# Performance work log

Measured on AMD Instinct MI355X. Metric: run time of the kernel, lower is better.

## Reference

```python
import jax, jax.numpy as jnp
import numpy as np

N = 100000

def _norm_edges(edge_index, n):
    # add self loops, compute symmetric GCN normalization
    loop = jnp.arange(n, dtype=edge_index.dtype)
    src = jnp.concatenate([edge_index[0], loop])
    dst = jnp.concatenate([edge_index[1], loop])
    deg = jax.ops.segment_sum(jnp.ones_like(dst, dtype=jnp.float32), dst, num_segments=n)
    dinv = jnp.where(deg > 0, deg ** -0.5, 0.0)
    norm = dinv[src] * dinv[dst]
    return src, dst, norm

def _gcn(x, W, b, src, dst, norm, n):
    h = x @ W  # [N, out]
    msg = h[src] * norm[:, None]
    return jax.ops.segment_sum(msg, dst, num_segments=n) + b

def setup_inputs() -> dict:
    key = jax.random.key(0)
    ks = jax.random.split(key, 20)
    E = 3200000
    d_in, d_out = 64, 64
    def w(k, i, o):
        return jax.random.normal(k, (i, o), dtype=jnp.float32) * (1.0 / np.sqrt(i))
    return {
        "x": jax.random.normal(ks[0], (N, d_in), dtype=jnp.float32),
        "t": jax.random.normal(ks[1], (N,), dtype=jnp.float32),
        "edge_index": jax.random.randint(ks[2], (2, E), 0, N, dtype=jnp.int64),
        "W1": w(ks[3], d_in + 1, 64), "b1": jnp.zeros((64,), jnp.float32),
        "W2": w(ks[4], 64, 128), "b2": jnp.zeros((128,), jnp.float32),
        "W3": w(ks[5], 128, 256), "b3": jnp.zeros((256,), jnp.float32),
        "W4": w(ks[6], 256, 128), "b4": jnp.zeros((128,), jnp.float32),
        "F1": w(ks[7], 128, 256), "c1": jnp.zeros((256,), jnp.float32),
        "F2": w(ks[8], 256, 128), "c2": jnp.zeros((128,), jnp.float32),
        "F3": w(ks[9], 128, d_out), "c3": jnp.zeros((d_out,), jnp.float32),
    }

def reference(x, t, edge_index, W1, b1, W2, b2, W3, b3, W4, b4, F1, c1, F2, c2, F3, c3):
    n = x.shape[0]
    src, dst, norm = _norm_edges(edge_index, n)
    h = jnp.concatenate([x, t[:, None]], axis=1)
    h = jax.nn.gelu(_gcn(h, W1, b1, src, dst, norm, n))
    h = jax.nn.gelu(_gcn(h, W2, b2, src, dst, norm, n))
    h = jax.nn.gelu(_gcn(h, W3, b3, src, dst, norm, n))
    h = jax.nn.gelu(_gcn(h, W4, b4, src, dst, norm, n))
    h = jax.nn.gelu(h @ F1 + c1)
    h = jax.nn.gelu(h @ F2 + c2)
    return h @ F3 + c3
```

## Files before the change

### kernel.cpp

```cpp
#include <hip/hip_runtime.h>

static constexpr int BLK = 256;

typedef double d2 __attribute__((ext_vector_type(2)));

__device__ __forceinline__ double gelu_d(double v){
  double u = 0.7978845608028654 * (v + 0.044715 * v * v * v);
  return 0.5 * v * (1.0 + tanh(u));
}

__global__ void zero_k(int* __restrict__ a, int n){
  int stride = gridDim.x * blockDim.x;
  for (int i = blockIdx.x*blockDim.x + threadIdx.x; i < n; i += stride) a[i] = 0;
}

__global__ void detect_k(const int* __restrict__ ei, int* __restrict__ flag){
  if (threadIdx.x == 0 && blockIdx.x == 0){
    int zeros = 0;
    for (int i = 0; i < 64; ++i) if (ei[2*i + 1] == 0) ++zeros;
    *flag = (zeros >= 48) ? 1 : 0;
  }
}

__global__ void count_k(const int* __restrict__ ei, int E, const int* __restrict__ flag,
                        int* __restrict__ cnt){
  int is64 = *flag;
  int stride = gridDim.x * blockDim.x;
  for (int e = blockIdx.x*blockDim.x + threadIdx.x; e < E; e += stride){
    int d = is64 ? ei[2*(E + e)] : ei[E + e];
    atomicAdd(&cnt[d], 1);
  }
}

__global__ void dinv_k(const int* __restrict__ cnt, double* __restrict__ dinv, int n){
  int i = blockIdx.x*blockDim.x + threadIdx.x;
  if (i < n){
    double deg = (double)(cnt[i] + 1);
    dinv[i] = 1.0 / sqrt(deg);
  }
}

__global__ __launch_bounds__(256)
void scanA_k(const int* __restrict__ cnt, int* __restrict__ partial, int n, int chunk){
  __shared__ int red[256];
  int b = blockIdx.x;
  int lo = b * chunk, hi = min(n, lo + chunk);
  int s = 0;
  for (int i = lo + threadIdx.x; i < hi; i += 256) s += cnt[i];
  red[threadIdx.x] = s; __syncthreads();
  for (int off = 128; off > 0; off >>= 1){
    if (threadIdx.x < off) red[threadIdx.x] += red[threadIdx.x + off];
    __syncthreads();
  }
  if (threadIdx.x == 0) partial[b] = red[0];
}

__global__ __launch_bounds__(256)
void scanB_k(int* __restrict__ partial, int nb){
  __shared__ int sd[256];
  int tid = threadIdx.x;
  int v = (tid < nb) ? partial[tid] : 0;
  sd[tid] = v; __syncthreads();
  for (int off = 1; off < 256; off <<= 1){
    int t = (tid >= off) ? sd[tid - off] : 0;
    __syncthreads();
    sd[tid] += t;
    __syncthreads();
  }
  if (tid < nb) partial[tid] = sd[tid] - v;
  if (tid == 255) partial[nb] = sd[255];
}

__global__ __launch_bounds__(256)
void scanC_k(const int* __restrict__ cnt, const int* __restrict__ partial,
             int* __restrict__ rp, int n, int chunk, int nb){
  __shared__ int sd[256];
  int b = blockIdx.x;
  int lo = b * chunk, hi = min(n, lo + chunk);
  int run = partial[b];
  for (int base = lo; base < hi; base += 256){
    int i = base + threadIdx.x;
    int v = (i < hi) ? cnt[i] : 0;
    sd[threadIdx.x] = v; __syncthreads();
    for (int off = 1; off < 256; off <<= 1){
      int t = (threadIdx.x >= off) ? sd[threadIdx.x - off] : 0;
      __syncthreads();
      sd[threadIdx.x] += t;
      __syncthreads();
    }
    if (i < hi) rp[i] = run + sd[threadIdx.x] - v;
    run += sd[255];
    __syncthreads();
  }
  if (b == 0 && threadIdx.x == 0) rp[n] = partial[nb];
}

__global__ void scatter_k(const int* __restrict__ ei, int E, const int* __restrict__ flag,
                          const int* __restrict__ rp, int* __restrict__ fill,
                          const double* __restrict__ dinv,
                          int* __restrict__ col, double* __restrict__ val){
  int is64 = *flag;
  int stride = gridDim.x * blockDim.x;
  for (int e = blockIdx.x*blockDim.x + threadIdx.x; e < E; e += stride){
    int s = is64 ? ei[2*e]       : ei[e];
    int d = is64 ? ei[2*(E + e)] : ei[E + e];
    int p = rp[d] + atomicAdd(&fill[d], 1);
    col[p] = s;
    if (val) val[p] = dinv[s];
  }
}

template<typename ST>
__global__ void concat_k(const float* __restrict__ x, const float* __restrict__ t,
                         ST* __restrict__ h0, int n){
  int total = n * 66;
  int stride = gridDim.x * blockDim.x;
  for (int idx = blockIdx.x*blockDim.x + threadIdx.x; idx < total; idx += stride){
    int row = idx / 66;
    int c = idx - row * 66;
    float v = (c < 64) ? x[row*64 + c] : (c == 64 ? t[row] : 0.0f);
    h0[idx] = (ST)v;
  }
}

template<typename ST>
__global__ __launch_bounds__(256, 2)
void gemm_k(const ST* __restrict__ A, int K, int lda,
            const float* __restrict__ W, int NOUT,
            const float* __restrict__ bias,
            ST* __restrict__ C, float* __restrict__ Cf,
            int n, int fuse)
{
  __shared__ __align__(16) double As[128][34];
  __shared__ __align__(16) double Ws[32][66];
  int row0 = blockIdx.x * 128;
  int col0 = blockIdx.y * 64;
  int tid = threadIdx.x;
  int tr = tid >> 4, tc = tid & 15;
  int c0 = 2 * tc;
  double acc[8][4] = {};
  int ktiles = (K + 31) / 32;
  for (int kt = 0; kt < ktiles; ++kt){
    int k0 = kt * 32;
    {
      int r  = tid >> 1;
      int kk = (tid & 1) * 16;
      int gr = row0 + r;
      if constexpr (sizeof(ST) == 8){
        if (gr < n){
          const double* Ap = (const double*)A + (size_t)gr * lda + k0 + kk;
          #pragma unroll
          for (int g = 0; g < 8; ++g){
            d2 v = *(const d2*)(Ap + 2*g);
            *(d2*)&As[r][kk + 2*g] = v;
          }
        } else {
          #pragma unroll
          for (int g = 0; g < 8; ++g){ d2 z = {0.0, 0.0}; *(d2*)&As[r][kk + 2*g] = z; }
        }
      } else {
        const ST* Ap = A + (size_t)gr * lda + k0 + kk;
        #pragma unroll
        for (int u = 0; u < 16; ++u){
          int kg = k0 + kk + u;
          As[r][kk + u] = (gr < n && kg < K) ? (double)Ap[u] : 0.0;
        }
      }
    }
    {
      int r = tid >> 3;
      int c = (tid & 7) * 8;
      int kg = k0 + r;
      if (kg < K){
        const float* Wp = W + (size_t)kg * NOUT + col0 + c;
        #pragma unroll
        for (int g = 0; g < 4; ++g){
          d2 v; v.x = (double)Wp[2*g]; v.y = (double)Wp[2*g + 1];
          *(d2*)&Ws[r][c + 2*g] = v;
        }
      } else {
        #pragma unroll
        for (int g = 0; g < 4; ++g){ d2 z = {0.0, 0.0}; *(d2*)&Ws[r][c + 2*g] = z; }
      }
    }
    __syncthreads();
    #pragma unroll
    for (int kk = 0; kk < 32; kk += 2){
      d2 w0a = *(const d2*)&Ws[kk    ][c0];
      d2 w0b = *(const d2*)&Ws[kk    ][c0 + 32];
      d2 w1a = *(const d2*)&Ws[kk + 1][c0];
      d2 w1b = *(const d2*)&Ws[kk + 1][c0 + 32];
      #pragma unroll
      for (int i = 0; i < 8; ++i){
        d2 av = *(const d2*)&As[tr + 16*i][kk];
        acc[i][0] = fma(av.x, w0a.x, acc[i][0]);
        acc[i][1] = fma(av.x, w0a.y, acc[i][1]);
        acc[i][2] = fma(av.x, w0b.x, acc[i][2]);
        acc[i][3] = fma(av.x, w0b.y, acc[i][3]);
        acc[i][0] = fma(av.y, w1a.x, acc[i][0]);
        acc[i][1] = fma(av.y, w1a.y, acc[i][1]);
        acc[i][2] = fma(av.y, w1b.x, acc[i][2]);
        acc[i][3] = fma(av.y, w1b.y, acc[i][3]);
      }
    }
    __syncthreads();
  }
  #pragma unroll
  for (int i = 0; i < 8; ++i){
    int r = row0 + tr + 16*i;
    if (r >= n) continue;
    #pragma unroll
    for (int j = 0; j < 4; ++j){
      int c = col0 + ((j < 2) ? (c0 + j) : (c0 + 30 + j));
      double v = acc[i][j];
      if (fuse){ v += (double)bias[c]; if (fuse == 1) v = gelu_d(v); }
      if (fuse == 2) __builtin_nontemporal_store((float)v, &Cf[(size_t)r * NOUT + c]);
      else           __builtin_nontemporal_store((ST)v,   &C [(size_t)r * NOUT + c]);
    }
  }
}

template<typename ST, int NC>
__global__ __launch_bounds__(256)
void agg_k(const ST* __restrict__ T, const int* __restrict__ rp,
           const int* __restrict__ col, const double* __restrict__ val,
           const double* __restrict__ dinv, const float* __restrict__ bias,
           ST* __restrict__ O, int n, int fuse)
{
  constexpr int DOUT = NC * 64;
  int w = (blockIdx.x * blockDim.x + threadIdx.x) >> 6;
  int lane = threadIdx.x & 63;
  if (w >= n) return;
  double dv = dinv[w];
  const ST* Ti = T + (size_t)w * DOUT;
  double acc[NC];
  #pragma unroll
  for (int c = 0; c < NC; ++c) acc[c] = dv * (double)Ti[lane + 64*c];
  int e  = rp[w];
  int e1 = rp[w + 1];
  if (val){
    for (; e + 4 <= e1; e += 4){
      int s0 = __builtin_nontemporal_load(&col[e]);
      int s1 = __builtin_nontemporal_load(&col[e+1]);
      int s2 = __builtin_nontemporal_load(&col[e+2]);
      int s3 = __builtin_nontemporal_load(&col[e+3]);
      double v0 = __builtin_nontemporal_load(&val[e]);
      double v1 = __builtin_nontemporal_load(&val[e+1]);
      double v2 = __builtin_nontemporal_load(&val[e+2]);
      double v3 = __builtin_nontemporal_load(&val[e+3]);
      const ST* T0 = T + (size_t)s0 * DOUT;
      const ST* T1 = T + (size_t)s1 * DOUT;
      const ST* T2 = T + (size_t)s2 * DOUT;
      const ST* T3 = T + (size_t)s3 * DOUT;
      double t0[NC], t1[NC], t2[NC], t3[NC];
      #pragma unroll
      for (int c = 0; c < NC; ++c){
        t0[c] = (double)T0[lane + 64*c];
        t1[c] = (double)T1[lane + 64*c];
        t2[c] = (double)T2[lane + 64*c];
        t3[c] = (double)T3[lane + 64*c];
      }
      #pragma unroll
      for (int c = 0; c < NC; ++c){
        acc[c] = fma(v0, t0[c], acc[c]);
        acc[c] = fma(v1, t1[c], acc[c]);
        acc[c] = fma(v2, t2[c], acc[c]);
        acc[c] = fma(v3, t3[c], acc[c]);
      }
    }
    for (; e < e1; ++e){
      int s = __builtin_nontemporal_load(&col[e]);
      double v = __builtin_nontemporal_load(&val[e]);
      const ST* Ts = T + (size_t)s * DOUT;
      #pragma unroll
      for (int c = 0; c < NC; ++c) acc[c] = fma(v, (double)Ts[lane + 64*c], acc[c]);
    }
  } else {
    for (; e < e1; ++e){
      int s = col[e];
      double v = dinv[s];
      const ST* Ts = T + (size_t)s * DOUT;
      #pragma unroll
      for (int c = 0; c < NC; ++c) acc[c] = fma(v, (double)Ts[lane + 64*c], acc[c]);
    }
  }
  ST* Oi = O + (size_t)w * DOUT;
  #pragma unroll
  for (int c = 0; c < NC; ++c){
    double v = dv * acc[c];
    if (fuse) v = gelu_d(v + (double)bias[lane + 64*c]);
    __builtin_nontemporal_store((ST)v, &Oi[lane + 64*c]);
  }
}

template<typename ST>
static void run_net(const float* x, const float* t,
                    const float* W1, const float* b1, const float* W2, const float* b2,
                    const float* W3, const float* b3, const float* W4, const float* b4,
                    const float* F1, const float* c1, const float* F2, const float* c2,
                    const float* F3, const float* c3,
                    ST* b256, ST* ba, ST* bb,
                    const int* rp, const int* col, const double* val, const double* dinv,
                    float* out, int N, hipStream_t stream)
{
  auto gemm = [&](const ST* A, int K, int lda, const float* W, int NOUT, const float* bias,
                  ST* C, float* Cf, int fuse){
    dim3 g((N + 127) / 128, NOUT / 64);
    gemm_k<ST><<<g, dim3(BLK), 0, stream>>>(A, K, lda, W, NOUT, bias, C, Cf, N, fuse);
  };
  int aggGrid = (N * 64 + BLK - 1) / BLK;
  auto agg64 = [&](const ST* T, const float* bias, ST* O, int fuse){
    agg_k<ST,1><<<dim3(aggGrid), dim3(BLK), 0, stream>>>(T, rp, col, val, dinv, bias, O, N, fuse);
  };
  auto agg128 = [&](const ST* T, const float* bias, ST* O, int fuse){
    agg_k<ST,2><<<dim3(aggGrid), dim3(BLK), 0, stream>>>(T, rp, col, val, dinv, bias, O, N, fuse);
  };

  concat_k<ST><<<dim3(1024), dim3(BLK), 0, stream>>>(x, t, ba, N);
  gemm(ba, 65, 66, W1, 64, nullptr, bb, nullptr, 0);
  agg64(bb, b1, ba, 1);
  agg64(ba, nullptr, bb, 0);
  gemm(bb, 64, 64, W2, 128, b2, ba, nullptr, 1);
  agg128(ba, nullptr, bb, 0);
  gemm(bb, 128, 128, W3, 256, b3, b256, nullptr, 1);
  gemm(b256, 256, 256, W4, 128, nullptr, ba, nullptr, 0);
  agg128(ba, b4, bb, 1);
  gemm(bb, 128, 128, F1, 256, c1, b256, nullptr, 1);
  gemm(b256, 256, 256, F2, 128, c2, ba, nullptr, 1);
  gemm(ba, 128, 128, F3, 64, c3, nullptr, out, 2);
}

extern "C" void kernel_launch(void* const* d_in, const int* in_sizes, int n_in,
                              void* d_out, int out_size, void* d_ws, size_t ws_size,
                              hipStream_t stream)
{
  const float* x  = (const float*)d_in[0];
  const float* t  = (const float*)d_in[1];
  const int*   ei = (const int*)d_in[2];
  const float* W1 = (const float*)d_in[3];  const float* b1 = (const float*)d_in[4];
  const float* W2 = (const float*)d_in[5];  const float* b2 = (const float*)d_in[6];
  const float* W3 = (const float*)d_in[7];  const float* b3 = (const float*)d_in[8];
  const float* W4 = (const float*)d_in[9];  const float* b4 = (const float*)d_in[10];
  const float* F1 = (const float*)d_in[11]; const float* c1 = (const float*)d_in[12];
  const float* F2 = (const float*)d_in[13]; const float* c2 = (const float*)d_in[14];
  const float* F3 = (const float*)d_in[15]; const float* c3 = (const float*)d_in[16];
  float* out = (float*)d_out;
  int N = in_sizes[0] / 64;
  int E = in_sizes[2] / 2;

  char* p = (char*)d_ws;
  auto alloc = [&](size_t b){ char* r = p; p += (b + 255) & ~(size_t)255; return (void*)r; };
  int*    flag    = (int*)alloc(4);
  int*    cnt     = (int*)alloc((size_t)N * 4);
  int*    fill    = (int*)alloc((size_t)N * 4);
  int*    rp      = (int*)alloc((size_t)(N + 1) * 4);
  int*    partial = (int*)alloc((size_t)257 * 4);
  int*    col     = (int*)alloc((size_t)E * 4);
  double* dinv    = (double*)alloc((size_t)N * 8);
  size_t base = (size_t)(p - (char*)d_ws);

  size_t slackB = 1024;
  size_t actElems = (size_t)N * 512;
  size_t valBytes = ((size_t)E * 8 + 255) & ~(size_t)255;
  bool f64val = ws_size >= base + valBytes + actElems * sizeof(double) + 3*slackB;
  bool f64ok  = f64val || ws_size >= base + actElems * sizeof(double) + 3*slackB;
  bool f32val = ws_size >= base + valBytes + actElems * sizeof(float) + 3*slackB;
  bool f32ok  = f32val || ws_size >= base + actElems * sizeof(float) + 3*slackB;
  if (!f32ok) return;

  double* val = nullptr;
  if ((f64ok && f64val) || (!f64ok && f32val)) val = (double*)alloc((size_t)E * 8);

  int nb = 256;
  int chunk = (N + nb - 1) / nb;
  zero_k<<<dim3(256), dim3(BLK), 0, stream>>>(cnt, N);
  zero_k<<<dim3(256), dim3(BLK), 0, stream>>>(fill, N);
  detect_k<<<1, 64, 0, stream>>>(ei, flag);
  count_k<<<dim3(4096), dim3(BLK), 0, stream>>>(ei, E, flag, cnt);
  dinv_k<<<dim3((N + BLK - 1) / BLK), dim3(BLK), 0, stream>>>(cnt, dinv, N);
  scanA_k<<<dim3(nb), dim3(256), 0, stream>>>(cnt, partial, N, chunk);
  scanB_k<<<dim3(1), dim3(256), 0, stream>>>(partial, nb);
  scanC_k<<<dim3(nb), dim3(256), 0, stream>>>(cnt, partial, rp, N, chunk, nb);
  scatter_k<<<dim3(4096), dim3(BLK), 0, stream>>>(ei, E, flag, rp, fill, dinv, col, val);

  if (f64ok){
    double* b256 = (double*)alloc((size_t)N * 256 * 8 + slackB);
    double* ba   = (double*)alloc((size_t)N * 128 * 8 + slackB);
    double* bb   = (double*)alloc((size_t)N * 128 * 8 + slackB);
    run_net<double>(x, t, W1, b1, W2, b2, W3, b3, W4, b4, F1, c1, F2, c2, F3, c3,
                    b256, ba, bb, rp, col, val, dinv, out, N, stream);
  } else {
    float* b256 = (float*)alloc((size_t)N * 256 * 4 + slackB);
    float* ba   = (float*)alloc((size_t)N * 128 * 4 + slackB);
    float* bb   = (float*)alloc((size_t)N * 128 * 4 + slackB);
    run_net<float>(x, t, W1, b1, W2, b2, W3, b3, W4, b4, F1, c1, F2, c2, F3, c3,
                   b256, ba, bb, rp, col, val, dinv, out, N, stream);
  }
}
```

Measured before the change: 2.525 ms.

## Register-prefetch next GEMM tile, XOR-swizzle A tile in LDS, raise occupancy hint

The FP64 GEMM kernel now loads the next k-tile of A and W into registers while computing on the current tile in LDS, overlapping global memory latency with FMA work. The A tile in shared memory uses an XOR swizzle on the column index to reduce LDS bank conflicts for the row-strided reads. The launch bounds hint goes from 2 to 3 blocks per CU. Prefetch registers (16 doubles plus 8 floats) add pressure that competes with the higher occupancy target and may cause spills.

```diff
diff --git a/kernel.cpp b/kernel.cpp
--- a/kernel.cpp
+++ b/kernel.cpp
@@ -124,66 +124,89 @@
 }
 
 template<typename ST>
-__global__ __launch_bounds__(256, 2)
+__global__ __launch_bounds__(256, 3)
 void gemm_k(const ST* __restrict__ A, int K, int lda,
             const float* __restrict__ W, int NOUT,
             const float* __restrict__ bias,
             ST* __restrict__ C, float* __restrict__ Cf,
             int n, int fuse)
 {
-  __shared__ __align__(16) double As[128][34];
+  __shared__ __align__(16) double As[128 * 34];
   __shared__ __align__(16) double Ws[32][66];
-  int row0 = blockIdx.x * 128;
-  int col0 = blockIdx.y * 64;
-  int tid = threadIdx.x;
-  int tr = tid >> 4, tc = tid & 15;
-  int c0 = 2 * tc;
+  const int row0 = blockIdx.x * 128;
+  const int col0 = blockIdx.y * 64;
+  const int tid = threadIdx.x;
+  const int tr = tid >> 4, tc = tid & 15;
+  const int c0 = 2 * tc;
+  const int rdx = 2 * (tr & 7);
   double acc[8][4] = {};
-  int ktiles = (K + 31) / 32;
-  for (int kt = 0; kt < ktiles; ++kt){
-    int k0 = kt * 32;
-    {
-      int r  = tid >> 1;
-      int kk = (tid & 1) * 16;
-      int gr = row0 + r;
-      if constexpr (sizeof(ST) == 8){
-        if (gr < n){
-          const double* Ap = (const double*)A + (size_t)gr * lda + k0 + kk;
-          #pragma unroll
-          for (int g = 0; g < 8; ++g){
-            d2 v = *(const d2*)(Ap + 2*g);
-            *(d2*)&As[r][kk + 2*g] = v;
-          }
-        } else {
-          #pragma unroll
-          for (int g = 0; g < 8; ++g){ d2 z = {0.0, 0.0}; *(d2*)&As[r][kk + 2*g] = z; }
-        }
-      } else {
-        const ST* Ap = A + (size_t)gr * lda + k0 + kk;
+
+  const int sar = tid >> 1;
+  const int sah = tid & 1;
+  const int arb = sar * 34;
+  const int arx = 2 * (sar & 7);
+  const int swr = tid >> 3;
+  const int swc = (tid & 7) * 8;
+
+  const int ktiles = (K + 31) / 32;
+
+  double ga[16];
+  float  gw[8];
+
+  auto loadA = [&](int k0){
+    int gr = row0 + sar;
+    if constexpr (sizeof(ST) == 8){
+      if (gr < n){
+        const double* Ap = (const double*)A + (size_t)gr * lda + k0 + sah * 16;
         #pragma unroll
-        for (int u = 0; u < 16; ++u){
-          int kg = k0 + kk + u;
-          As[r][kk + u] = (gr < n && kg < K) ? (double)Ap[u] : 0.0;
-        }
-      }
-    }
-    {
-      int r = tid >> 3;
-      int c = (tid & 7) * 8;
-      int kg = k0 + r;
-      if (kg < K){
-        const float* Wp = W + (size_t)kg * NOUT + col0 + c;
-        #pragma unroll
-        for (int g = 0; g < 4; ++g){
-          d2 v; v.x = (double)Wp[2*g]; v.y = (double)Wp[2*g + 1];
-          *(d2*)&Ws[r][c + 2*g] = v;
+        for (int g = 0; g < 8; ++g){
+          d2 v = *(const d2*)(Ap + 2*g);
+          ga[2*g] = v.x; ga[2*g+1] = v.y;
         }
       } else {
         #pragma unroll
-        for (int g = 0; g < 4; ++g){ d2 z = {0.0, 0.0}; *(d2*)&Ws[r][c + 2*g] = z; }
+        for (int u = 0; u < 16; ++u) ga[u] = 0.0;
       }
-    }
-    __syncthreads();
+    } else {
+      const ST* Ap = A + (size_t)gr * lda + k0 + sah * 16;
+      #pragma unroll
+      for (int u = 0; u < 16; ++u){
+        int kg = k0 + sah * 16 + u;
+        ga[u] = (gr < n && kg < K) ? (double)Ap[u] : 0.0;
+      }
+    }
+  };
+  auto loadW = [&](int k0){
+    int kg = k0 + swr;
+    if (kg < K){
+      const float* Wp = W + (size_t)kg * NOUT + col0 + swc;
+      #pragma unroll
+      for (int g = 0; g < 8; ++g) gw[g] = Wp[g];
+    } else {
+      #pragma unroll
+      for (int g = 0; g < 8; ++g) gw[g] = 0.0f;
+    }
+  };
+
+  loadA(0);
+  loadW(0);
+
+  for (int kt = 0; kt < ktiles; ++kt){
+    #pragma unroll
+    for (int g = 0; g < 8; ++g){
+      d2 v; v.x = ga[2*g]; v.y = ga[2*g+1];
+      *(d2*)&As[arb + ((sah * 16 + 2*g) ^ arx)] = v;
+    }
+    #pragma unroll
+    for (int g = 0; g < 4; ++g){
+      d2 v; v.x = (double)gw[2*g]; v.y = (double)gw[2*g+1];
+      *(d2*)&Ws[swr][swc + 2*g] = v;
+    }
+    __syncthreads();
+    if (kt + 1 < ktiles){
+      loadA((kt + 1) * 32);
+      loadW((kt + 1) * 32);
+    }
     #pragma unroll
     for (int kk = 0; kk < 32; kk += 2){
       d2 w0a = *(const d2*)&Ws[kk    ][c0];
@@ -192,7 +215,7 @@
       d2 w1b = *(const d2*)&Ws[kk + 1][c0 + 32];
       #pragma unroll
       for (int i = 0; i < 8; ++i){
-        d2 av = *(const d2*)&As[tr + 16*i][kk];
+        d2 av = *(const d2*)&As[(tr + 16*i) * 34 + (kk ^ rdx)];
         acc[i][0] = fma(av.x, w0a.x, acc[i][0]);
         acc[i][1] = fma(av.x, w0a.y, acc[i][1]);
         acc[i][2] = fma(av.x, w0b.x, acc[i][2]);
```

New measurement: 2.595 ms. 2.8% more time.
